# Optimization experiments

Hardware: AMD Instinct MI355X
Metric: run time of the kernel (lower is better)

The kernel has to match this reference:

```python
import jax, jax.numpy as jnp
import numpy as np

EPS = 1e-12  # keras K.l2_normalize epsilon


def _l2_normalize(v, axis):
    return v * jax.lax.rsqrt(jnp.maximum(jnp.sum(v * v, axis=axis, keepdims=True), EPS))


def setup_inputs() -> dict:
    key = jax.random.key(0)
    k1, k2, k3, k4 = jax.random.split(key, 4)
    B, T, D, K, O = 32, 1024, 512, 64, 1024
    x = jax.random.normal(k1, (B, T, D), dtype=jnp.float32)
    weight = jax.random.normal(k2, (D, K), dtype=jnp.float32) * (1.0 / np.sqrt(D))
    bias = jnp.zeros((K,), dtype=jnp.float32)
    centers = jax.random.normal(k3, (K, D), dtype=jnp.float32)
    reduc_dim = jax.random.normal(k4, (D * K, O), dtype=jnp.float32) * 0.01
    return {"x": x, "weight": weight, "bias": bias, "centers": centers, "reduc_dim": reduc_dim}


def reference(x, weight, bias, centers, reduc_dim):
    # x: [B,T,D], weight: [D,K], bias: [K]
    # soft assignment: softmax over centers
    a = jax.nn.softmax(jnp.einsum('btd,dk->btk', x, weight) + bias, axis=-1)  # [B,T,K]
    # aggregate descriptors per center: batch_dot over time axis -> [B,K,D]
    x_agg = jnp.einsum('btk,btd->bkd', a, x)
    # total soft weight per center: [B,K]
    sum_w = jnp.sum(a, axis=1)
    # residual vs centers, broadcast: [B,K,D]
    full = x_agg - sum_w[:, :, None] * centers[None, :, :]
    # intra-normalize per center vector
    full = _l2_normalize(full, axis=-1)
    B = x.shape[0]
    full = full.reshape(B, -1)  # [B, K*D]
    full = _l2_normalize(full, axis=-1)
    return full @ reduc_dim  # [B, output_dim]
```

## Files before the change

kernel.cpp:

```cpp
#include <hip/hip_runtime.h>
#include <math.h>

#define TT 1024
#define DD 512
#define KK 64
#define OO 1024
#define EPSF 1e-12f

typedef __attribute__((ext_vector_type(8))) short bf16x8;
typedef __attribute__((ext_vector_type(4))) float f32x4;

__device__ __forceinline__ ushort f2bf(float f) {
  unsigned u = __float_as_uint(f);
  u = (u + 0x7FFFu + ((u >> 16) & 1u)) >> 16;
  return (ushort)u;
}
__device__ __forceinline__ float bf2f(ushort h) {
  return __uint_as_float(((unsigned)h) << 16);
}


__global__ __launch_bounds__(256) void nv_k0(const float* __restrict__ w,
                                             ushort* __restrict__ whT,
                                             float* __restrict__ sum_w) {
  int idx = blockIdx.x * 256 + threadIdx.x;
  if (idx < 32768) {
    int d = idx >> 6, k = idx & 63;
    whT[(size_t)k * DD + d] = f2bf(w[idx]);
  } else if (idx < 32768 + 2048) {
    sum_w[idx - 32768] = 0.f;
  }
}

__global__ __launch_bounds__(256) void nv_k12(
    const float* __restrict__ x, const ushort* __restrict__ whT,
    const float* __restrict__ bias, float* __restrict__ xaggP,
    float* __restrict__ sum_w) {
  const int tsp = blockIdx.x, b = blockIdx.y;
  const int t0 = tsp * 128;
  const int tid = threadIdx.x;
  const int wave = tid >> 6, lane = tid & 63, l15 = lane & 15, q = lane >> 4;

  __shared__ ushort xs[128 * 64];
  __shared__ ushort wsm[64 * 64];
  __shared__ ushort aTl[64 * 128];
  __shared__ ushort xsT[64 * 128];

  f32x4 acc[2][4];
#pragma unroll
  for (int mt = 0; mt < 2; ++mt)
#pragma unroll
    for (int nt = 0; nt < 4; ++nt)
#pragma unroll
      for (int r = 0; r < 4; ++r) acc[mt][nt][r] = 0.f;

  for (int dc = 0; dc < DD; dc += 64) {
    __syncthreads();
#pragma unroll
    for (int it = 0; it < 4; ++it) {
      int gi = it * 256 + tid;
      int t = gi >> 3, gd = gi & 7;
      const float* px = x + (size_t)(b * TT + t0 + t) * DD + dc + gd * 8;
      float4 v0 = *(const float4*)px;
      float4 v1 = *(const float4*)(px + 4);
      bf16x8 pk;
      pk[0] = (short)f2bf(v0.x); pk[1] = (short)f2bf(v0.y);
      pk[2] = (short)f2bf(v0.z); pk[3] = (short)f2bf(v0.w);
      pk[4] = (short)f2bf(v1.x); pk[5] = (short)f2bf(v1.y);
      pk[6] = (short)f2bf(v1.z); pk[7] = (short)f2bf(v1.w);
      *(bf16x8*)(xs + t * 64 + ((gd ^ (t & 7)) << 3)) = pk;
    }
#pragma unroll
    for (int it = 0; it < 2; ++it) {
      int gi = it * 256 + tid;
      int k = gi >> 3, gd = gi & 7;
      bf16x8 v = *(const bf16x8*)(whT + (size_t)k * DD + dc + gd * 8);
      *(bf16x8*)(wsm + k * 64 + ((gd ^ (k & 7)) << 3)) = v;
    }
    __syncthreads();
#pragma unroll
    for (int kc = 0; kc < 2; ++kc) {
      int gq = kc * 4 + q;
      bf16x8 bfv[4];
#pragma unroll
      for (int nt = 0; nt < 4; ++nt) {
        int k = nt * 16 + l15;
        bfv[nt] = *(const bf16x8*)(wsm + k * 64 + ((gq ^ (k & 7)) << 3));
      }
#pragma unroll
      for (int mt = 0; mt < 2; ++mt) {
        int t = wave * 32 + mt * 16 + l15;
        bf16x8 af = *(const bf16x8*)(xs + t * 64 + ((gq ^ (t & 7)) << 3));
#pragma unroll
        for (int nt = 0; nt < 4; ++nt)
          acc[mt][nt] = __builtin_amdgcn_mfma_f32_16x16x32_bf16(af, bfv[nt], acc[mt][nt], 0, 0, 0);
      }
    }
  }

  float bia[4];
#pragma unroll
  for (int nt = 0; nt < 4; ++nt) bia[nt] = bias[nt * 16 + l15];

  ushort au[2][4][4];
  float sw[4] = {0.f, 0.f, 0.f, 0.f};
#pragma unroll
  for (int mt = 0; mt < 2; ++mt)
#pragma unroll
    for (int r = 0; r < 4; ++r) {
      float l[4];
#pragma unroll
      for (int nt = 0; nt < 4; ++nt) l[nt] = acc[mt][nt][r] + bia[nt];
      float m = fmaxf(fmaxf(l[0], l[1]), fmaxf(l[2], l[3]));
#pragma unroll
      for (int s = 1; s <= 8; s <<= 1) m = fmaxf(m, __shfl_xor(m, s));
      float e[4];
#pragma unroll
      for (int nt = 0; nt < 4; ++nt) e[nt] = __expf(l[nt] - m);
      float ssum = e[0] + e[1] + e[2] + e[3];
#pragma unroll
      for (int s = 1; s <= 8; s <<= 1) ssum += __shfl_xor(ssum, s);
      float inv = 1.f / ssum;
#pragma unroll
      for (int nt = 0; nt < 4; ++nt) {
        ushort u = f2bf(e[nt] * inv);
        au[mt][nt][r] = u;
        sw[nt] += bf2f(u);
      }
    }
#pragma unroll
  for (int nt = 0; nt < 4; ++nt) {
    float s = sw[nt];
    s += __shfl_xor(s, 16);
    s += __shfl_xor(s, 32);
    if (q == 0) atomicAdd(sum_w + b * KK + nt * 16 + l15, s);
  }
#pragma unroll
  for (int mt = 0; mt < 2; ++mt)
#pragma unroll
    for (int nt = 0; nt < 4; ++nt)
#pragma unroll
      for (int r = 0; r < 4; ++r) {
        int k = nt * 16 + l15;
        int t = wave * 32 + mt * 16 + q * 4 + r;
        aTl[k * 128 + (((t >> 3) ^ (k & 15)) << 3) + (t & 7)] = au[mt][nt][r];
      }
  __syncthreads();

  bf16x8 afB[4][4];
#pragma unroll
  for (int mk = 0; mk < 4; ++mk)
#pragma unroll
    for (int ks = 0; ks < 4; ++ks) {
      int k = mk * 16 + l15;
      int g = ks * 4 + q;
      afB[mk][ks] = *(const bf16x8*)(aTl + k * 128 + ((g ^ (k & 15)) << 3));
    }

  for (int dc = 0; dc < DD; dc += 64) {
    __syncthreads();
#pragma unroll
    for (int it = 0; it < 8; ++it) {
      int fi = it * 256 + tid;
      int t = fi >> 4, dq = fi & 15;
      float4 v = *(const float4*)(x + (size_t)(b * TT + t0 + t) * DD + dc + dq * 4);
      int tg = t >> 3;
      float vv[4] = {v.x, v.y, v.z, v.w};
#pragma unroll
      for (int i = 0; i < 4; ++i) {
        int d = dq * 4 + i;
        xsT[d * 128 + ((tg ^ (d & 15)) << 3) + (t & 7)] = f2bf(vv[i]);
      }
    }
    __syncthreads();
    f32x4 accB[4];
#pragma unroll
    for (int mk = 0; mk < 4; ++mk)
#pragma unroll
      for (int r = 0; r < 4; ++r) accB[mk][r] = 0.f;
#pragma unroll
    for (int ks = 0; ks < 4; ++ks) {
      int d = wave * 16 + l15;
      int g = ks * 4 + q;
      bf16x8 bfv = *(const bf16x8*)(xsT + d * 128 + ((g ^ (d & 15)) << 3));
#pragma unroll
      for (int mk = 0; mk < 4; ++mk)
        accB[mk] = __builtin_amdgcn_mfma_f32_16x16x32_bf16(afB[mk][ks], bfv, accB[mk], 0, 0, 0);
    }
#pragma unroll
    for (int mk = 0; mk < 4; ++mk)
#pragma unroll
      for (int r = 0; r < 4; ++r) {
        int k = mk * 16 + q * 4 + r;
        xaggP[(size_t)((tsp * 32 + b) * KK + k) * DD + dc + wave * 16 + l15] = accB[mk][r];
      }
  }
}

__global__ __launch_bounds__(128) void nv_k3a(
    const float* __restrict__ xaggP, float* __restrict__ full,
    const float* __restrict__ centers, const float* __restrict__ sum_w,
    float* __restrict__ s1) {
  const int k = blockIdx.x, b = blockIdx.y;
  const int tid = threadIdx.x;
  const float sw = sum_w[b * KK + k];
  float4 v = make_float4(0.f, 0.f, 0.f, 0.f);
#pragma unroll
  for (int sp = 0; sp < 8; ++sp) {
    float4 p = *((const float4*)(xaggP + (size_t)((sp * 32 + b) * KK + k) * DD) + tid);
    v.x += p.x; v.y += p.y; v.z += p.z; v.w += p.w;
  }
  float4 c = *((const float4*)(centers + (size_t)k * DD) + tid);
  v.x = fmaf(-sw, c.x, v.x);
  v.y = fmaf(-sw, c.y, v.y);
  v.z = fmaf(-sw, c.z, v.z);
  v.w = fmaf(-sw, c.w, v.w);
  *((float4*)(full + (size_t)(b * KK + k) * DD) + tid) = v;
  float ss = v.x * v.x + v.y * v.y + v.z * v.z + v.w * v.w;
#pragma unroll
  for (int s = 1; s <= 32; s <<= 1) ss += __shfl_xor(ss, s);
  __shared__ float red[2];
  if ((tid & 63) == 0) red[tid >> 6] = ss;
  __syncthreads();
  if (tid == 0) s1[b * KK + k] = red[0] + red[1];
}

__global__ __launch_bounds__(64) void nv_k3b(const float* __restrict__ s1,
                                             float* __restrict__ scale) {
  const int b = blockIdx.x, k = threadIdx.x;
  float r = s1[b * KK + k];
  float d1 = fmaxf(r, EPSF);
  float s2 = r / d1;
#pragma unroll
  for (int s = 1; s <= 32; s <<= 1) s2 += __shfl_xor(s2, s);
  scale[b * KK + k] = rsqrtf(d1) * rsqrtf(fmaxf(s2, EPSF));
}

__global__ __launch_bounds__(256) void nv_k3c(const float* __restrict__ full,
                                              const float* __restrict__ scale,
                                              float* __restrict__ fullT) {
  const int k = blockIdx.x, d0 = blockIdx.y * 128;
  const int tid = threadIdx.x;
  __shared__ float ls[32 * 132];

#pragma unroll
  for (int it = 0; it < 4; ++it) {
    int fi = it * 256 + tid;
    int b = fi >> 5, dg = fi & 31;
    float sc = scale[b * KK + k];
    float4 v = *((const float4*)(full + (size_t)(b * KK + k) * DD + d0) + dg);
    v.x *= sc; v.y *= sc; v.z *= sc; v.w *= sc;
    *(float4*)(ls + b * 132 + dg * 4) = v;
  }
  __syncthreads();
#pragma unroll
  for (int it = 0; it < 4; ++it) {
    int fo = it * 256 + tid;
    int d = fo >> 3, bq = fo & 7;
    float4 v;
    v.x = ls[(bq * 4 + 0) * 132 + d];
    v.y = ls[(bq * 4 + 1) * 132 + d];
    v.z = ls[(bq * 4 + 2) * 132 + d];
    v.w = ls[(bq * 4 + 3) * 132 + d];
    *(float4*)(fullT + (size_t)(k * DD + d0 + d) * 32 + bq * 4) = v;
  }
}

__global__ __launch_bounds__(256) void nv_k4(
    const float* __restrict__ fullT, const float* __restrict__ reduc,
    float* __restrict__ outP) {
  const int strip = blockIdx.x;
  const int ksp = blockIdx.y;
  const int tid = threadIdx.x;
  const int wave = tid >> 6, lane = tid & 63;
  const int c0 = strip * 256 + lane * 4;
  const int kblk = ksp * 256;

  __shared__ float fst[256 * 32];

#pragma unroll
  for (int it = 0; it < 8; ++it) {
    int f4 = it * 256 + tid;
    *(float4*)(fst + f4 * 4) = *(const float4*)(fullT + (size_t)kblk * 32 + f4 * 4);
  }
  __syncthreads();

  float4 acc[32];
#pragma unroll
  for (int b = 0; b < 32; ++b) acc[b] = make_float4(0.f, 0.f, 0.f, 0.f);

  const int kw = wave * 64;
  for (int kk = 0; kk < 64; kk += 4) {
    float4 rv[4];
#pragma unroll
    for (int j = 0; j < 4; ++j)
      rv[j] = *(const float4*)(reduc + (size_t)(kblk + kw + kk + j) * OO + c0);
#pragma unroll
    for (int j = 0; j < 4; ++j) {
      const int kl = kw + kk + j;
#pragma unroll
      for (int b4 = 0; b4 < 8; ++b4) {
        float4 fv = *(const float4*)(fst + kl * 32 + b4 * 4);
        acc[b4 * 4 + 0].x = fmaf(fv.x, rv[j].x, acc[b4 * 4 + 0].x);
        acc[b4 * 4 + 0].y = fmaf(fv.x, rv[j].y, acc[b4 * 4 + 0].y);
        acc[b4 * 4 + 0].z = fmaf(fv.x, rv[j].z, acc[b4 * 4 + 0].z);
        acc[b4 * 4 + 0].w = fmaf(fv.x, rv[j].w, acc[b4 * 4 + 0].w);
        acc[b4 * 4 + 1].x = fmaf(fv.y, rv[j].x, acc[b4 * 4 + 1].x);
        acc[b4 * 4 + 1].y = fmaf(fv.y, rv[j].y, acc[b4 * 4 + 1].y);
        acc[b4 * 4 + 1].z = fmaf(fv.y, rv[j].z, acc[b4 * 4 + 1].z);
        acc[b4 * 4 + 1].w = fmaf(fv.y, rv[j].w, acc[b4 * 4 + 1].w);
        acc[b4 * 4 + 2].x = fmaf(fv.z, rv[j].x, acc[b4 * 4 + 2].x);
        acc[b4 * 4 + 2].y = fmaf(fv.z, rv[j].y, acc[b4 * 4 + 2].y);
        acc[b4 * 4 + 2].z = fmaf(fv.z, rv[j].z, acc[b4 * 4 + 2].z);
        acc[b4 * 4 + 2].w = fmaf(fv.z, rv[j].w, acc[b4 * 4 + 2].w);
        acc[b4 * 4 + 3].x = fmaf(fv.w, rv[j].x, acc[b4 * 4 + 3].x);
        acc[b4 * 4 + 3].y = fmaf(fv.w, rv[j].y, acc[b4 * 4 + 3].y);
        acc[b4 * 4 + 3].z = fmaf(fv.w, rv[j].z, acc[b4 * 4 + 3].z);
        acc[b4 * 4 + 3].w = fmaf(fv.w, rv[j].w, acc[b4 * 4 + 3].w);
      }
    }
  }

  __syncthreads();
  for (int w = 0; w < 4; ++w) {
    if (wave == w) {
      if (w == 0) {
#pragma unroll
        for (int b = 0; b < 32; ++b)
          *(float4*)(fst + b * 256 + lane * 4) = acc[b];
      } else {
#pragma unroll
        for (int b = 0; b < 32; ++b) {
          float4 v = *(float4*)(fst + b * 256 + lane * 4);
          v.x += acc[b].x; v.y += acc[b].y; v.z += acc[b].z; v.w += acc[b].w;
          *(float4*)(fst + b * 256 + lane * 4) = v;
        }
      }
    }
    __syncthreads();
  }

#pragma unroll
  for (int it = 0; it < 8; ++it) {
    int f4 = it * 256 + tid;
    int b = f4 >> 6, cg = f4 & 63;
    *(float4*)(outP + ((size_t)(ksp * 32 + b) * OO) + strip * 256 + cg * 4) =
        *(const float4*)(fst + b * 256 + cg * 4);
  }
}

__global__ __launch_bounds__(128) void nv_k5(const float* __restrict__ outP,
                                             float* __restrict__ out) {
  const int idx = blockIdx.x * 128 + threadIdx.x;
  float s = 0.f;
#pragma unroll 8
  for (int sp = 0; sp < 128; ++sp) s += outP[(size_t)sp * 32768 + idx];
  out[idx] = s;
}

extern "C" void kernel_launch(void* const* d_in, const int* in_sizes, int n_in,
                              void* d_out, int out_size, void* d_ws, size_t ws_size,
                              hipStream_t stream) {
  const float* x = (const float*)d_in[0];
  const float* weight = (const float*)d_in[1];
  const float* bias = (const float*)d_in[2];
  const float* centers = (const float*)d_in[3];
  const float* reduc = (const float*)d_in[4];
  float* out = (float*)d_out;
  float* ws = (float*)d_ws;

  float* xaggP = ws;
  float* full = ws + 8388608;
  float* fullT = ws + 9437184;
  float* outP = ws + 10485760;
  ushort* whT = (ushort*)(ws + 14680064);
  float* sum_w = ws + 14696448;
  float* s1 = sum_w + 2048;
  float* scale = sum_w + 4096;

  nv_k0<<<136, 256, 0, stream>>>(weight, whT, sum_w);
  nv_k12<<<dim3(8, 32), 256, 0, stream>>>(x, whT, bias, xaggP, sum_w);
  nv_k3a<<<dim3(64, 32), 128, 0, stream>>>(xaggP, full, centers, sum_w, s1);
  nv_k3b<<<32, 64, 0, stream>>>(s1, scale);
  nv_k3c<<<dim3(64, 4), 256, 0, stream>>>(full, scale, fullT);
  nv_k4<<<dim3(4, 128), 256, 0, stream>>>(fullT, reduc, outP);
  nv_k5<<<256, 128, 0, stream>>>(outP, out);
}
```

Before: 288.1 us.

## Read x once into LDS as transposed bf16 tile, reuse for both GEMMs

The fused assignment/aggregation kernel previously read each x tile from global memory twice, once for the logits GEMM and again for the aggregation GEMM. Now each of 8 waves (512 threads) loads its 16 rows of x straight into registers for the first MFMA and also writes them transposed as bf16 into a 128KB LDS tile covering all of D. The second GEMM then runs entirely from LDS, and weight fragments are read directly from global memory instead of being staged. This halves global traffic on x and removes per-chunk barriers, but the large LDS footprint limits the CU to one block and the per-element transposed stores may bank-conflict.

```diff
diff --git a/kernel.cpp b/kernel.cpp
--- a/kernel.cpp
+++ b/kernel.cpp
@@ -32,7 +32,7 @@
   }
 }
 
-__global__ __launch_bounds__(256) void nv_k12(
+__global__ __launch_bounds__(512) void nv_k12(
     const float* __restrict__ x, const ushort* __restrict__ whT,
     const float* __restrict__ bias, float* __restrict__ xaggP,
     float* __restrict__ sum_w) {
@@ -41,60 +41,42 @@
   const int tid = threadIdx.x;
   const int wave = tid >> 6, lane = tid & 63, l15 = lane & 15, q = lane >> 4;
 
-  __shared__ ushort xs[128 * 64];
-  __shared__ ushort wsm[64 * 64];
+  __shared__ ushort xT[512 * 128];
   __shared__ ushort aTl[64 * 128];
-  __shared__ ushort xsT[64 * 128];
-
-  f32x4 acc[2][4];
-#pragma unroll
-  for (int mt = 0; mt < 2; ++mt)
-#pragma unroll
-    for (int nt = 0; nt < 4; ++nt)
-#pragma unroll
-      for (int r = 0; r < 4; ++r) acc[mt][nt][r] = 0.f;
+
+  f32x4 acc[4];
+#pragma unroll
+  for (int nt = 0; nt < 4; ++nt)
+#pragma unroll
+    for (int r = 0; r < 4; ++r) acc[nt][r] = 0.f;
+
+  const int trow = wave * 16 + l15;
+  const float* xrow = x + (size_t)(b * TT + t0 + trow) * DD;
+  const int tg = trow >> 3, tlo = trow & 7;
 
   for (int dc = 0; dc < DD; dc += 64) {
-    __syncthreads();
-#pragma unroll
-    for (int it = 0; it < 4; ++it) {
-      int gi = it * 256 + tid;
-      int t = gi >> 3, gd = gi & 7;
-      const float* px = x + (size_t)(b * TT + t0 + t) * DD + dc + gd * 8;
-      float4 v0 = *(const float4*)px;
-      float4 v1 = *(const float4*)(px + 4);
-      bf16x8 pk;
-      pk[0] = (short)f2bf(v0.x); pk[1] = (short)f2bf(v0.y);
-      pk[2] = (short)f2bf(v0.z); pk[3] = (short)f2bf(v0.w);
-      pk[4] = (short)f2bf(v1.x); pk[5] = (short)f2bf(v1.y);
-      pk[6] = (short)f2bf(v1.z); pk[7] = (short)f2bf(v1.w);
-      *(bf16x8*)(xs + t * 64 + ((gd ^ (t & 7)) << 3)) = pk;
-    }
-#pragma unroll
-    for (int it = 0; it < 2; ++it) {
-      int gi = it * 256 + tid;
-      int k = gi >> 3, gd = gi & 7;
-      bf16x8 v = *(const bf16x8*)(whT + (size_t)k * DD + dc + gd * 8);
-      *(bf16x8*)(wsm + k * 64 + ((gd ^ (k & 7)) << 3)) = v;
-    }
-    __syncthreads();
 #pragma unroll
     for (int kc = 0; kc < 2; ++kc) {
-      int gq = kc * 4 + q;
+      const int dbase = dc + kc * 32 + q * 8;
+      float4 v0 = *(const float4*)(xrow + dbase);
+      float4 v1 = *(const float4*)(xrow + dbase + 4);
+      bf16x8 af;
+      af[0] = (short)f2bf(v0.x); af[1] = (short)f2bf(v0.y);
+      af[2] = (short)f2bf(v0.z); af[3] = (short)f2bf(v0.w);
+      af[4] = (short)f2bf(v1.x); af[5] = (short)f2bf(v1.y);
+      af[6] = (short)f2bf(v1.z); af[7] = (short)f2bf(v1.w);
+#pragma unroll
+      for (int j = 0; j < 8; ++j) {
+        const int d = dbase + j;
+        xT[d * 128 + ((tg ^ (d & 15)) << 3) + tlo] = (ushort)af[j];
+      }
       bf16x8 bfv[4];
 #pragma unroll
-      for (int nt = 0; nt < 4; ++nt) {
-        int k = nt * 16 + l15;
-        bfv[nt] = *(const bf16x8*)(wsm + k * 64 + ((gq ^ (k & 7)) << 3));
-      }
-#pragma unroll
-      for (int mt = 0; mt < 2; ++mt) {
-        int t = wave * 32 + mt * 16 + l15;
-        bf16x8 af = *(const bf16x8*)(xs + t * 64 + ((gq ^ (t & 7)) << 3));
-#pragma unroll
-        for (int nt = 0; nt < 4; ++nt)
-          acc[mt][nt] = __builtin_amdgcn_mfma_f32_16x16x32_bf16(af, bfv[nt], acc[mt][nt], 0, 0, 0);
-      }
+      for (int nt = 0; nt < 4; ++nt)
+        bfv[nt] = *(const bf16x8*)(whT + (size_t)(nt * 16 + l15) * DD + dbase);
+#pragma unroll
+      for (int nt = 0; nt < 4; ++nt)
+        acc[nt] = __builtin_amdgcn_mfma_f32_16x16x32_bf16(af, bfv[nt], acc[nt], 0, 0, 0);
     }
   }
 
@@ -102,32 +84,30 @@
 #pragma unroll
   for (int nt = 0; nt < 4; ++nt) bia[nt] = bias[nt * 16 + l15];
 
-  ushort au[2][4][4];
+  ushort au[4][4];
   float sw[4] = {0.f, 0.f, 0.f, 0.f};
 #pragma unroll
-  for (int mt = 0; mt < 2; ++mt)
-#pragma unroll
-    for (int r = 0; r < 4; ++r) {
-      float l[4];
-#pragma unroll
-      for (int nt = 0; nt < 4; ++nt) l[nt] = acc[mt][nt][r] + bia[nt];
-      float m = fmaxf(fmaxf(l[0], l[1]), fmaxf(l[2], l[3]));
-#pragma unroll
-      for (int s = 1; s <= 8; s <<= 1) m = fmaxf(m, __shfl_xor(m, s));
-      float e[4];
-#pragma unroll
-      for (int nt = 0; nt < 4; ++nt) e[nt] = __expf(l[nt] - m);
-      float ssum = e[0] + e[1] + e[2] + e[3];
-#pragma unroll
-      for (int s = 1; s <= 8; s <<= 1) ssum += __shfl_xor(ssum, s);
-      float inv = 1.f / ssum;
-#pragma unroll
-      for (int nt = 0; nt < 4; ++nt) {
-        ushort u = f2bf(e[nt] * inv);
-        au[mt][nt][r] = u;
-        sw[nt] += bf2f(u);
-      }
-    }
+  for (int r = 0; r < 4; ++r) {
+    float l[4];
+#pragma unroll
+    for (int nt = 0; nt < 4; ++nt) l[nt] = acc[nt][r] + bia[nt];
+    float m = fmaxf(fmaxf(l[0], l[1]), fmaxf(l[2], l[3]));
+#pragma unroll
+    for (int s = 1; s <= 8; s <<= 1) m = fmaxf(m, __shfl_xor(m, s));
+    float e[4];
+#pragma unroll
+    for (int nt = 0; nt < 4; ++nt) e[nt] = __expf(l[nt] - m);
+    float ssum = e[0] + e[1] + e[2] + e[3];
+#pragma unroll
+    for (int s = 1; s <= 8; s <<= 1) ssum += __shfl_xor(ssum, s);
+    float inv = 1.f / ssum;
+#pragma unroll
+    for (int nt = 0; nt < 4; ++nt) {
+      ushort u = f2bf(e[nt] * inv);
+      au[nt][r] = u;
+      sw[nt] += bf2f(u);
+    }
+  }
 #pragma unroll
   for (int nt = 0; nt < 4; ++nt) {
     float s = sw[nt];
@@ -136,65 +116,54 @@
     if (q == 0) atomicAdd(sum_w + b * KK + nt * 16 + l15, s);
   }
 #pragma unroll
-  for (int mt = 0; mt < 2; ++mt)
-#pragma unroll
-    for (int nt = 0; nt < 4; ++nt)
+  for (int nt = 0; nt < 4; ++nt)
+#pragma unroll
+    for (int r = 0; r < 4; ++r) {
+      const int k = nt * 16 + l15;
+      const int t = wave * 16 + q * 4 + r;
+      aTl[k * 128 + (((t >> 3) ^ (k & 15)) << 3) + (t & 7)] = au[nt][r];
+    }
+  __syncthreads();
+
+  f32x4 accB[4][4];
+#pragma unroll
+  for (int mk = 0; mk < 4; ++mk)
+#pragma unroll
+    for (int nd = 0; nd < 4; ++nd)
+#pragma unroll
+      for (int r = 0; r < 4; ++r) accB[mk][nd][r] = 0.f;
+
+#pragma unroll
+  for (int kc = 0; kc < 4; ++kc) {
+    const int g = kc * 4 + q;
+    bf16x8 afr[4], bfr[4];
+#pragma unroll
+    for (int mk = 0; mk < 4; ++mk) {
+      const int k = mk * 16 + l15;
+      afr[mk] = *(const bf16x8*)(aTl + k * 128 + ((g ^ (k & 15)) << 3));
+    }
+#pragma unroll
+    for (int nd = 0; nd < 4; ++nd) {
+      const int d = wave * 64 + nd * 16 + l15;
+      bfr[nd] = *(const bf16x8*)(xT + d * 128 + ((g ^ (d & 15)) << 3));
+    }
+#pragma unroll
+    for (int mk = 0; mk < 4; ++mk)
+#pragma unroll
+      for (int nd = 0; nd < 4; ++nd)
+        accB[mk][nd] =
+            __builtin_amdgcn_mfma_f32_16x16x32_bf16(afr[mk], bfr[nd], accB[mk][nd], 0, 0, 0);
+  }
+#pragma unroll
+  for (int mk = 0; mk < 4; ++mk)
+#pragma unroll
+    for (int nd = 0; nd < 4; ++nd)
 #pragma unroll
       for (int r = 0; r < 4; ++r) {
-        int k = nt * 16 + l15;
-        int t = wave * 32 + mt * 16 + q * 4 + r;
-        aTl[k * 128 + (((t >> 3) ^ (k & 15)) << 3) + (t & 7)] = au[mt][nt][r];
+        const int k = mk * 16 + q * 4 + r;
+        const int d = wave * 64 + nd * 16 + l15;
+        xaggP[(size_t)((tsp * 32 + b) * KK + k) * DD + d] = accB[mk][nd][r];
       }
-  __syncthreads();
-
-  bf16x8 afB[4][4];
-#pragma unroll
-  for (int mk = 0; mk < 4; ++mk)
-#pragma unroll
-    for (int ks = 0; ks < 4; ++ks) {
-      int k = mk * 16 + l15;
-      int g = ks * 4 + q;
-      afB[mk][ks] = *(const bf16x8*)(aTl + k * 128 + ((g ^ (k & 15)) << 3));
-    }
-
-  for (int dc = 0; dc < DD; dc += 64) {
-    __syncthreads();
-#pragma unroll
-    for (int it = 0; it < 8; ++it) {
-      int fi = it * 256 + tid;
-      int t = fi >> 4, dq = fi & 15;
-      float4 v = *(const float4*)(x + (size_t)(b * TT + t0 + t) * DD + dc + dq * 4);
-      int tg = t >> 3;
-      float vv[4] = {v.x, v.y, v.z, v.w};
-#pragma unroll
-      for (int i = 0; i < 4; ++i) {
-        int d = dq * 4 + i;
-        xsT[d * 128 + ((tg ^ (d & 15)) << 3) + (t & 7)] = f2bf(vv[i]);
-      }
-    }
-    __syncthreads();
-    f32x4 accB[4];
-#pragma unroll
-    for (int mk = 0; mk < 4; ++mk)
-#pragma unroll
-      for (int r = 0; r < 4; ++r) accB[mk][r] = 0.f;
-#pragma unroll
-    for (int ks = 0; ks < 4; ++ks) {
-      int d = wave * 16 + l15;
-      int g = ks * 4 + q;
-      bf16x8 bfv = *(const bf16x8*)(xsT + d * 128 + ((g ^ (d & 15)) << 3));
-#pragma unroll
-      for (int mk = 0; mk < 4; ++mk)
-        accB[mk] = __builtin_amdgcn_mfma_f32_16x16x32_bf16(afB[mk][ks], bfv, accB[mk], 0, 0, 0);
-    }
-#pragma unroll
-    for (int mk = 0; mk < 4; ++mk)
-#pragma unroll
-      for (int r = 0; r < 4; ++r) {
-        int k = mk * 16 + q * 4 + r;
-        xaggP[(size_t)((tsp * 32 + b) * KK + k) * DD + dc + wave * 16 + l15] = accB[mk][r];
-      }
-  }
 }
 
 __global__ __launch_bounds__(128) void nv_k3a(
@@ -379,7 +348,7 @@
   float* scale = sum_w + 4096;
 
   nv_k0<<<136, 256, 0, stream>>>(weight, whT, sum_w);
-  nv_k12<<<dim3(8, 32), 256, 0, stream>>>(x, whT, bias, xaggP, sum_w);
+  nv_k12<<<dim3(8, 32), 512, 0, stream>>>(x, whT, bias, xaggP, sum_w);
   nv_k3a<<<dim3(64, 32), 128, 0, stream>>>(xaggP, full, centers, sum_w, s1);
   nv_k3b<<<32, 64, 0, stream>>>(s1, scale);
   nv_k3c<<<dim3(64, 4), 256, 0, stream>>>(full, scale, fullT);
```

New measurement: 277.8 us. 1.04x faster.
